# Optimization experiments

Hardware: AMD Instinct MI355X
Metric: run time of the kernel (lower is better)

Reference implementation:

```python
import jax, jax.numpy as jnp
import numpy as np

B, IN_C, H, W = 2, 256, 128, 128
KQ = 128            # kq_dim
K_LOCAL = 5         # subsample_local_ksize -> 25 local samples
S = 32              # subsample_num_samples (25 local + 7 random global)
STRIDES = (1, 2, 4) # levels 2, 3, 4


def _local_inds(h, w, k):
    # create_local_ind_buffer: flat index of the KxK window around each pixel,
    # coordinates clamped at the border (padding by replication).
    off = np.arange(k) - k // 2
    ii = np.clip(np.arange(h)[:, None] + off[None, :], 0, h - 1)  # [h,k]
    jj = np.clip(np.arange(w)[:, None] + off[None, :], 0, w - 1)  # [w,k]
    inds = ii[:, None, :, None] * w + jj[None, :, None, :]        # [h,w,k,k]
    return inds.reshape(h * w, k * k)


def setup_inputs() -> dict:
    key = jax.random.key(0)
    ks = jax.random.split(key, 4)
    rng = np.random.RandomState(0)
    inp = {
        'feats': jax.random.normal(ks[0], (B, IN_C, H, W), jnp.float32),
        'conv_w': jax.random.normal(ks[1], (KQ, IN_C, 3, 3), jnp.float32) * 0.02,
        'conv_b': jnp.zeros((KQ,), jnp.float32),
        'key_w': jax.random.normal(ks[2], (KQ, KQ), jnp.float32) * 0.05,
        'key_b': jnp.zeros((KQ,), jnp.float32),
        'query_w': jax.random.normal(ks[3], (KQ, KQ), jnp.float32) * 0.05,
        'query_b': jnp.zeros((KQ,), jnp.float32),
    }
    for lvl, s in zip((2, 3, 4), STRIDES):
        h, w = H // s, W // s
        n = h * w
        loc = np.broadcast_to(_local_inds(h, w, K_LOCAL)[None], (B, n, K_LOCAL * K_LOCAL))
        glob = rng.randint(0, n, size=(B, n, S - K_LOCAL * K_LOCAL))
        inp['sample_inds_%d' % lvl] = jnp.asarray(np.concatenate([loc, glob], -1), jnp.int32)
    return inp


def _pool(x, s):
    # utils.downscale_tensor: average-pool by the level stride
    if s == 1:
        return x
    b, c, h, w = x.shape
    return x.reshape(b, c, h // s, s, w // s, s).mean(axis=(3, 5))


def _level_logits(key_f, query_f, stride, inds):
    k = _pool(key_f, stride)
    q = _pool(query_f, stride)
    b, c, h, w = k.shape
    k = k.reshape(b, c, h * w).transpose(0, 2, 1)   # [B,N,C]
    q = q.reshape(b, c, h * w).transpose(0, 2, 1)   # [B,N,C]
    gk = k[jnp.arange(b)[:, None, None], inds]      # gather keys -> [B,N,S,C]
    # (gathered_query * gathered_key).sum(-1); query gather at node_inds is identity
    return jnp.einsum('bnc,bnsc->bns', q, gk) * (c ** -0.5)


def reference(feats, conv_w, conv_b, key_w, key_b, query_w, query_b,
              sample_inds_2, sample_inds_3, sample_inds_4):
    x = jax.lax.conv_general_dilated(
        feats, conv_w, (1, 1), 'SAME',
        dimension_numbers=('NCHW', 'OIHW', 'NCHW')) + conv_b[None, :, None, None]
    keys = jnp.einsum('bchw,kc->bkhw', x, key_w) + key_b[None, :, None, None]
    queries = jnp.einsum('bchw,kc->bkhw', x, query_w) + query_b[None, :, None, None]
    logits = [
        _level_logits(keys, queries, s, i)
        for s, i in zip(STRIDES, (sample_inds_2, sample_inds_3, sample_inds_4))
    ]
    # subsample_logits for levels 2/3/4, concatenated along the node dim
    return jnp.concatenate(logits, axis=1)  # [B, 16384+4096+1024, S]
```

## Files before the change

### kernel.cpp

```cpp
#include <hip/hip_runtime.h>
#include <cstddef>
#include <cstdint>

typedef __attribute__((ext_vector_type(8))) short short8;
typedef __attribute__((ext_vector_type(4))) float f32x4;

namespace {
constexpr int B_   = 2;
constexpr int HW   = 16384;
constexpr int NTOT = 21504;
constexpr float SCALE = 0.088388347648318447f;
}

__device__ __forceinline__ unsigned short f2bf(float f) {
    unsigned u = __builtin_bit_cast(unsigned, f);
    u += 0x7fffu + ((u >> 16) & 1u);
    return (unsigned short)(u >> 16);
}
__device__ __forceinline__ float bf2f(unsigned short h) {
    return __builtin_bit_cast(float, (unsigned)h << 16);
}
__device__ __forceinline__ float blo(unsigned u) {
    return __builtin_bit_cast(float, u << 16);
}
__device__ __forceinline__ float bhi(unsigned u) {
    return __builtin_bit_cast(float, u & 0xffff0000u);
}
__device__ __forceinline__ void gload_lds16(const void* g, void* l) {
    __builtin_amdgcn_global_load_lds(
        (const __attribute__((address_space(1))) void*)g,
        (__attribute__((address_space(3))) void*)l, 16, 0, 0);
}

__global__ __launch_bounds__(64) void zb_k(unsigned short* __restrict__ fpm)
{
    int bid = blockIdx.x;
    int b = bid >= 516;
    int i = bid - b * 516;
    int yy, xx;
    if (i < 130)      { yy = 0;       xx = i; }
    else if (i < 260) { yy = 129;     xx = i - 130; }
    else if (i < 388) { yy = i - 259; xx = 0; }
    else              { yy = i - 387; xx = 129; }
    ((unsigned long long*)fpm)[((size_t)(b * 130 + yy) * 130 + xx) * 64 + threadIdx.x] = 0ull;
}

__global__ __launch_bounds__(256) void t_k(
    const float* __restrict__ feats, unsigned short* __restrict__ fpm)
{
    __shared__ unsigned short ls[256 * 72];
    const int tid = threadIdx.x;
    const int b    = blockIdx.x >> 8;
    const int rem  = blockIdx.x & 255;
    const int y    = rem >> 1;
    const int gx0  = (rem & 1) << 6;

    const int cs = tid >> 4, x0 = (tid & 15) << 2;
#pragma unroll
    for (int j = 0; j < 16; ++j) {
        int c = (j << 4) + cs;
        float4 v = *(const float4*)&feats[(((size_t)b * 256 + c) << 14) + (y << 7) + gx0 + x0];
        uint2 pk;
        pk.x = (unsigned)f2bf(v.x) | ((unsigned)f2bf(v.y) << 16);
        pk.y = (unsigned)f2bf(v.z) | ((unsigned)f2bf(v.w) << 16);
        *(uint2*)&ls[c * 72 + x0] = pk;
    }
    __syncthreads();

    const int x = tid >> 2, q = tid & 3;
    unsigned short* orow = fpm +
        (((size_t)(b * 130 + y + 1) * 130) + 1 + gx0 + x) * 256 + (q << 6);
#pragma unroll
    for (int u = 0; u < 8; ++u) {
        int c0 = (q << 6) + (u << 3);
        unsigned w0 = (unsigned)ls[(c0 + 0) * 72 + x] | ((unsigned)ls[(c0 + 1) * 72 + x] << 16);
        unsigned w1 = (unsigned)ls[(c0 + 2) * 72 + x] | ((unsigned)ls[(c0 + 3) * 72 + x] << 16);
        unsigned w2 = (unsigned)ls[(c0 + 4) * 72 + x] | ((unsigned)ls[(c0 + 5) * 72 + x] << 16);
        unsigned w3 = (unsigned)ls[(c0 + 6) * 72 + x] | ((unsigned)ls[(c0 + 7) * 72 + x] << 16);
        uint4 o; o.x = w0; o.y = w1; o.z = w2; o.w = w3;
        *(uint4*)(orow + (u << 3)) = o;
    }
}

__global__ __launch_bounds__(256) void prep_w_k(
    const float* __restrict__ cw, const float* __restrict__ kw,
    const float* __restrict__ qw, unsigned short* __restrict__ wp)
{
    __shared__ float cvec[128][4];
    const int tid = threadIdx.x;
    const int g = blockIdx.x;
    for (int idx = tid; idx < 512; idx += 256) {
        int j = idx >> 2, q = idx & 3;
        int pair = (g << 2) + q;
        int c = pair / 9, tap = pair - c * 9;
        cvec[j][q] = cw[j * 2304 + c * 9 + tap];
    }
    __syncthreads();
    const int oc = tid & 127, isQ = tid >> 7;
    const float* wrow = (isQ ? qw : kw) + oc * 128;
    float acc0 = 0.f, acc1 = 0.f, acc2 = 0.f, acc3 = 0.f;
    for (int j = 0; j < 128; ++j) {
        float wv = wrow[j];
        acc0 += wv * cvec[j][0]; acc1 += wv * cvec[j][1];
        acc2 += wv * cvec[j][2]; acc3 += wv * cvec[j][3];
    }
    float accs[4] = {acc0, acc1, acc2, acc3};
#pragma unroll
    for (int q = 0; q < 4; ++q) {
        int pair = (g << 2) + q;
        int c = pair / 9, tap = pair - c * 9;
        int chunk = c >> 5, kg = (c >> 3) & 3, i = c & 7;
        int nf = (isQ << 3) + (oc >> 4);
        int lane = (kg << 4) + (oc & 15);
        wp[((size_t)(((chunk * 9 + tap) << 4) + nf) << 9) + (lane << 3) + i] = f2bf(accs[q]);
    }
}

__global__ __launch_bounds__(256) void prep_bias_k(
    const float* __restrict__ cb, const float* __restrict__ kw,
    const float* __restrict__ qw, const float* __restrict__ kb,
    const float* __restrict__ qb, float* __restrict__ bias)
{
    __shared__ float cbv[128];
    const int tid = threadIdx.x;
    if (tid < 128) cbv[tid] = cb[tid];
    __syncthreads();
    const int oc = tid & 127, isQ = tid >> 7;
    const float* wrow = (isQ ? qw : kw) + oc * 128;
    float a = isQ ? qb[oc] : kb[oc];
    for (int j = 0; j < 128; ++j) a += wrow[j] * cbv[j];
    bias[tid] = a;
}

__global__ __launch_bounds__(256, 2) void conv2_k(
    const unsigned short* __restrict__ fpm, const unsigned short* __restrict__ wp,
    const float* __restrict__ kqbias, unsigned short* __restrict__ kT,
    unsigned short* __restrict__ qT)
{
    __shared__ __align__(16) unsigned char abuf[2][7168];
    const int tid = threadIdx.x;
    const int w = tid >> 6, lane = tid & 63;
    const int raw = blockIdx.x;
    const int bid = ((raw & 7) << 6) + (raw >> 3);
    const int b = bid >> 8, tile = bid & 255;
    const int ty0 = (tile >> 4) << 3, tx0 = (tile & 15) << 3;
    const int r = lane & 15, g = lane >> 4;

    const int sp_sub = lane >> 2, sp_o = (lane & 3) << 4;
    const int pbase = (((r >> 3) * 10) + (r & 7)) * 64 + (g << 4);
    const unsigned char* wpB = (const unsigned char*)wp + ((w << 2) << 10) + (lane << 4);

    f32x4 acc[4][4];
#pragma unroll
    for (int mi = 0; mi < 4; ++mi)
#pragma unroll
        for (int ni = 0; ni < 4; ++ni) acc[mi][ni] = (f32x4){0.f, 0.f, 0.f, 0.f};

    auto stage = [&](int chunk, int buf) {
#pragma unroll
        for (int k = 0; k < 2; ++k) {
            int i = w + (k << 2);
            if (i < 7) {
                int pl0 = (i << 4) + sp_sub;
                int y = (pl0 * 6554) >> 16;
                int x = pl0 - y * 10;
                const unsigned char* src = (const unsigned char*)fpm +
                    (((size_t)((b * 130 + ty0 + y) * 130 + tx0 + x)) << 9) +
                    (chunk << 6) + sp_o;
                gload_lds16(src, &abuf[buf][i << 10]);
            }
        }
    };

    stage(0, 0);
    __syncthreads();

    for (int chunk = 0; chunk < 8; ++chunk) {
        const unsigned char* ab = abuf[chunk & 1];
        if (chunk < 7) stage(chunk + 1, (chunk + 1) & 1);
        const unsigned char* wbase = wpB + (size_t)chunk * 147456;

        short8 breg[2][4];
#pragma unroll
        for (int ni = 0; ni < 4; ++ni)
            breg[0][ni] = *(const short8*)(wbase + (ni << 10));

#pragma unroll
        for (int tap = 0; tap < 9; ++tap) {
            const int dy = tap / 3, dx = tap % 3;
            const int cur = tap & 1, nxt = cur ^ 1;
            if (tap < 8) {
#pragma unroll
                for (int ni = 0; ni < 4; ++ni)
                    breg[nxt][ni] = *(const short8*)(wbase + (tap + 1) * 16384 + (ni << 10));
            }
            short8 af[4];
#pragma unroll
            for (int mi = 0; mi < 4; ++mi)
                af[mi] = *(const short8*)(ab + pbase + (((2 * mi + dy) * 10 + dx) << 6));
#pragma unroll
            for (int mi = 0; mi < 4; ++mi)
#pragma unroll
                for (int ni = 0; ni < 4; ++ni)
                    acc[mi][ni] = __builtin_amdgcn_mfma_f32_16x16x32_bf16(
                        af[mi], breg[cur][ni], acc[mi][ni], 0, 0, 0);
        }
        __syncthreads();
    }

    const int col = lane & 15;
    const int mrow0 = g << 2;
#pragma unroll
    for (int ni = 0; ni < 4; ++ni) {
        int nf = (w << 2) + ni;
        unsigned short* dst = (nf < 8) ? kT : qT;
        int oc = ((nf & 7) << 4) + col;
        float bias = kqbias[(nf < 8 ? 0 : 128) + oc];
#pragma unroll
        for (int mi = 0; mi < 4; ++mi)
#pragma unroll
            for (int reg = 0; reg < 4; ++reg) {
                int m = mrow0 + reg;
                int ly = 2 * mi + (m >> 3), lx = m & 7;
                int gp = ((ty0 + ly) << 7) + tx0 + lx;
                dst[(((size_t)b << 14) + gp) * 128 + oc] = f2bf(acc[mi][ni][reg] + bias);
            }
    }
}

__global__ __launch_bounds__(256) void pool_all_k(
    const unsigned short* __restrict__ kT1, const unsigned short* __restrict__ qT1,
    unsigned short* __restrict__ kT2, unsigned short* __restrict__ qT2,
    unsigned short* __restrict__ kT3, unsigned short* __restrict__ qT3)
{
    const int bid = blockIdx.x;
    const unsigned short* src; unsigned short* dst;
    int s, pwshift, np, b, bx;
    if (bid < 2048) {
        int j = bid & 1023;
        src = (bid < 1024) ? kT1 : qT1; dst = (bid < 1024) ? kT2 : qT2;
        s = 2; pwshift = 6; np = 4096; b = j >> 9; bx = j & 511;
    } else {
        int j = (bid - 2048) & 255;
        src = (bid < 2304) ? kT1 : qT1; dst = (bid < 2304) ? kT3 : qT3;
        s = 4; pwshift = 5; np = 1024; b = j >> 7; bx = j & 127;
    }
    const int tid = threadIdx.x;
    const int pp = (bx << 3) + (tid >> 5);
    const int c4 = (tid & 31) << 2;
    const int ppy = pp >> pwshift, ppx = pp & ((1 << pwshift) - 1);
    float a0 = 0.f, a1 = 0.f, a2 = 0.f, a3 = 0.f;
    for (int sy = 0; sy < s; ++sy)
        for (int sx = 0; sx < s; ++sx) {
            int sp = ((ppy * s + sy) << 7) + ppx * s + sx;
            ushort4 v = *(const ushort4*)(src + (((size_t)b << 14) + sp) * 128 + c4);
            a0 += bf2f(v.x); a1 += bf2f(v.y); a2 += bf2f(v.z); a3 += bf2f(v.w);
        }
    const float inv = 1.f / (float)(s * s);
    ushort4 o;
    o.x = f2bf(a0 * inv); o.y = f2bf(a1 * inv);
    o.z = f2bf(a2 * inv); o.w = f2bf(a3 * inv);
    *(ushort4*)(dst + ((size_t)b * np + pp) * 128 + c4) = o;
}

__global__ __launch_bounds__(512, 2) void gdot_all_k(
    const unsigned short* __restrict__ qT1, const unsigned short* __restrict__ kT1,
    const unsigned short* __restrict__ qT2, const unsigned short* __restrict__ kT2,
    const unsigned short* __restrict__ qT3, const unsigned short* __restrict__ kT3,
    const int* __restrict__ i2, const int* __restrict__ i3, const int* __restrict__ i4,
    float* __restrict__ out)
{
    __shared__ __align__(16) unsigned char kwin[144 * 256];

    const int raw = blockIdx.x;
    const int bid = (raw & 7) * 84 + (raw >> 3);

    const unsigned short *qT, *kT;
    const int* inds;
    int n, wshift, tpbsh, twsh, off;
    if (bid < 512) {
        qT = qT1; kT = kT1; inds = i2; n = 16384; wshift = 7; tpbsh = 8; twsh = 4; off = 0;
    } else if (bid < 640) {
        qT = qT2; kT = kT2; inds = i3; n = 4096;  wshift = 6; tpbsh = 6; twsh = 3; off = 16384;
    } else {
        qT = qT3; kT = kT3; inds = i4; n = 1024;  wshift = 5; tpbsh = 4; twsh = 2; off = 20480;
    }
    const int lb   = bid - ((bid < 512) ? 0 : (bid < 640) ? 512 : 640);
    const int b    = lb >> tpbsh;
    const int tile = lb & ((1 << tpbsh) - 1);
    const int ty0  = (tile >> twsh) << 3;
    const int tx0  = (tile & ((1 << twsh) - 1)) << 3;
    const int W    = 1 << wshift, Wm1 = W - 1;
    const int ry0  = ty0 - 2, cx0 = tx0 - 2;

    const int tid   = threadIdx.x;
    const int pxl   = tid >> 3;
    const int slice = tid & 7;
    const int py = pxl >> 3, px = pxl & 7;
    const int nid = ((ty0 + py) << wshift) + tx0 + px;

    for (int idx = tid; idx < 2304; idx += 512) {
        int slot = idx >> 4, w16 = idx & 15;
        int sy = ry0 + slot / 12, sx = cx0 + slot % 12;
        sy = min(max(sy, 0), Wm1); sx = min(max(sx, 0), Wm1);
        uint4 v = *(const uint4*)(kT + ((size_t)(b * n + (sy << wshift) + sx) * 128) + (w16 << 3));
        *(uint4*)&kwin[slot * 256 + ((w16 ^ (slot & 7)) << 4)] = v;
    }

    float qr[16];
    {
        const uint4* qp = (const uint4*)(qT + ((size_t)(b * n + nid) * 128) + (slice << 4));
        uint4 q0 = qp[0], q1 = qp[1];
        qr[0] = blo(q0.x); qr[1] = bhi(q0.x); qr[2] = blo(q0.y); qr[3] = bhi(q0.y);
        qr[4] = blo(q0.z); qr[5] = bhi(q0.z); qr[6] = blo(q0.w); qr[7] = bhi(q0.w);
        qr[8] = blo(q1.x); qr[9] = bhi(q1.x); qr[10] = blo(q1.y); qr[11] = bhi(q1.y);
        qr[12] = blo(q1.z); qr[13] = bhi(q1.z); qr[14] = blo(q1.w); qr[15] = bhi(q1.w);
    }
    __syncthreads();

    const int* irow = inds + ((size_t)(b * n + nid) << 5);
    const int w2 = slice << 1;
    float* orow = out + (((size_t)b * NTOT + off + nid) << 5);

    for (int s = 0; s < 32; ++s) {
        int ind = irow[s];
        uint4 k0, k1;
        if (s < 25) {
            int iy = ind >> wshift, ix = ind & Wm1;
            int slot = (iy - ry0) * 12 + (ix - cx0);
            int sw = slot & 7;
            const unsigned char* base = kwin + slot * 256;
            k0 = *(const uint4*)(base + ((w2 ^ sw) << 4));
            k1 = *(const uint4*)(base + (((w2 + 1) ^ sw) << 4));
        } else {
            const uint4* kp = (const uint4*)(kT + ((size_t)(b * n + ind) * 128) + (slice << 4));
            k0 = kp[0]; k1 = kp[1];
        }
        float a = qr[0] * blo(k0.x) + qr[1] * bhi(k0.x)
                + qr[2] * blo(k0.y) + qr[3] * bhi(k0.y)
                + qr[4] * blo(k0.z) + qr[5] * bhi(k0.z)
                + qr[6] * blo(k0.w) + qr[7] * bhi(k0.w)
                + qr[8] * blo(k1.x) + qr[9] * bhi(k1.x)
                + qr[10] * blo(k1.y) + qr[11] * bhi(k1.y)
                + qr[12] * blo(k1.z) + qr[13] * bhi(k1.z)
                + qr[14] * blo(k1.w) + qr[15] * bhi(k1.w);
        a += __shfl_xor(a, 1);
        a += __shfl_xor(a, 2);
        a += __shfl_xor(a, 4);
        if (slice == 0) orow[s] = a * SCALE;
    }
}

extern "C" void kernel_launch(void* const* d_in, const int* in_sizes, int n_in,
                              void* d_out, int out_size, void* d_ws, size_t ws_size,
                              hipStream_t stream)
{
    const float* feats = (const float*)d_in[0];
    const float* cw    = (const float*)d_in[1];
    const float* cb    = (const float*)d_in[2];
    const float* kw    = (const float*)d_in[3];
    const float* kb    = (const float*)d_in[4];
    const float* qw    = (const float*)d_in[5];
    const float* qb    = (const float*)d_in[6];
    const int*   i2    = (const int*)d_in[7];
    const int*   i3    = (const int*)d_in[8];
    const int*   i4    = (const int*)d_in[9];
    float* out = (float*)d_out;

    char* ws = (char*)d_ws;
    unsigned short* wp   = (unsigned short*)ws;
    float*          bias = (float*)(ws + 1179648);
    unsigned short* fpm  = (unsigned short*)(ws + 1180672);
    unsigned short* kT1  = (unsigned short*)(ws + 18624512);
    unsigned short* qT1  = kT1 + 4194304;
    unsigned short* kT2  = qT1 + 4194304;
    unsigned short* qT2  = kT2 + 1048576;
    unsigned short* kT3  = qT2 + 1048576;
    unsigned short* qT3  = kT3 + 262144;

    zb_k<<<dim3(1032), 64, 0, stream>>>(fpm);
    t_k<<<dim3(512), 256, 0, stream>>>(feats, fpm);
    prep_w_k<<<dim3(576), 256, 0, stream>>>(cw, kw, qw, wp);
    prep_bias_k<<<dim3(1), 256, 0, stream>>>(cb, kw, qw, kb, qb, bias);
    conv2_k<<<dim3(512), 256, 0, stream>>>(fpm, wp, bias, kT1, qT1);
    pool_all_k<<<dim3(2560), 256, 0, stream>>>(kT1, qT1, kT2, qT2, kT3, qT3);
    gdot_all_k<<<dim3(672), 512, 0, stream>>>(qT1, kT1, qT2, kT2, qT3, kT3,
                                              i2, i3, i4, out);
}
```

Measured before the change: 212.2 us.

## Fuse pooling into conv epilogue, merge prep kernels, fold border zeroing into transpose

The separate border-zeroing, bias-prep and pooling kernels are removed. Zero padding moves into a new transpose kernel that reads the input directly without an LDS stage, and bias prep becomes an extra block of the weight-prep kernel. The conv kernel now stages its output tile in LDS, writes coalesced rows, and computes the 2x and 4x average pools from that tile. The gather-dot kernel preloads its index row and the random-global keys into registers and writes results as float4 from every slice. The weight register double-buffering, block swizzle and the 2-blocks-per-SM bound on gdot are also dropped, and the large extra LDS buffer in conv may lower occupancy.

```diff
diff --git a/kernel.cpp b/kernel.cpp
--- a/kernel.cpp
+++ b/kernel.cpp
@@ -26,68 +26,68 @@
 __device__ __forceinline__ float bhi(unsigned u) {
     return __builtin_bit_cast(float, u & 0xffff0000u);
 }
+__device__ __forceinline__ unsigned pk2(float a, float b) {
+    return (unsigned)f2bf(a) | ((unsigned)f2bf(b) << 16);
+}
 __device__ __forceinline__ void gload_lds16(const void* g, void* l) {
     __builtin_amdgcn_global_load_lds(
         (const __attribute__((address_space(1))) void*)g,
         (__attribute__((address_space(3))) void*)l, 16, 0, 0);
 }
 
-__global__ __launch_bounds__(64) void zb_k(unsigned short* __restrict__ fpm)
-{
-    int bid = blockIdx.x;
-    int b = bid >= 516;
-    int i = bid - b * 516;
-    int yy, xx;
-    if (i < 130)      { yy = 0;       xx = i; }
-    else if (i < 260) { yy = 129;     xx = i - 130; }
-    else if (i < 388) { yy = i - 259; xx = 0; }
-    else              { yy = i - 387; xx = 129; }
-    ((unsigned long long*)fpm)[((size_t)(b * 130 + yy) * 130 + xx) * 64 + threadIdx.x] = 0ull;
-}
-
-__global__ __launch_bounds__(256) void t_k(
+__global__ __launch_bounds__(256) void t2_k(
     const float* __restrict__ feats, unsigned short* __restrict__ fpm)
 {
-    __shared__ unsigned short ls[256 * 72];
     const int tid = threadIdx.x;
-    const int b    = blockIdx.x >> 8;
-    const int rem  = blockIdx.x & 255;
-    const int y    = rem >> 1;
-    const int gx0  = (rem & 1) << 6;
-
-    const int cs = tid >> 4, x0 = (tid & 15) << 2;
-#pragma unroll
-    for (int j = 0; j < 16; ++j) {
-        int c = (j << 4) + cs;
-        float4 v = *(const float4*)&feats[(((size_t)b * 256 + c) << 14) + (y << 7) + gx0 + x0];
-        uint2 pk;
-        pk.x = (unsigned)f2bf(v.x) | ((unsigned)f2bf(v.y) << 16);
-        pk.y = (unsigned)f2bf(v.z) | ((unsigned)f2bf(v.w) << 16);
-        *(uint2*)&ls[c * 72 + x0] = pk;
-    }
-    __syncthreads();
-
-    const int x = tid >> 2, q = tid & 3;
-    unsigned short* orow = fpm +
-        (((size_t)(b * 130 + y + 1) * 130) + 1 + gx0 + x) * 256 + (q << 6);
-#pragma unroll
-    for (int u = 0; u < 8; ++u) {
-        int c0 = (q << 6) + (u << 3);
-        unsigned w0 = (unsigned)ls[(c0 + 0) * 72 + x] | ((unsigned)ls[(c0 + 1) * 72 + x] << 16);
-        unsigned w1 = (unsigned)ls[(c0 + 2) * 72 + x] | ((unsigned)ls[(c0 + 3) * 72 + x] << 16);
-        unsigned w2 = (unsigned)ls[(c0 + 4) * 72 + x] | ((unsigned)ls[(c0 + 5) * 72 + x] << 16);
-        unsigned w3 = (unsigned)ls[(c0 + 6) * 72 + x] | ((unsigned)ls[(c0 + 7) * 72 + x] << 16);
-        uint4 o; o.x = w0; o.y = w1; o.z = w2; o.w = w3;
-        *(uint4*)(orow + (u << 3)) = o;
-    }
-}
-
-__global__ __launch_bounds__(256) void prep_w_k(
+    const int lane = tid & 63, cg = tid >> 6;
+    const int y = blockIdx.x >> 1, xseg = blockIdx.x & 1;
+    const int b = blockIdx.y;
+    const int x = (xseg << 6) + lane;
+    const bool inter = (y >= 1 && y <= 128);
+    const float* src = feats + (((size_t)b * 256) << 14) + ((y - 1) << 7) + x;
+    unsigned short* orow = fpm + ((size_t)(b * 130 + y) * 130 + 1 + x) * 256;
+
+#pragma unroll
+    for (int it = 0; it < 8; ++it) {
+        const int c0 = (it << 5) + (cg << 3);
+        uint4 v = {0u, 0u, 0u, 0u};
+        if (inter) {
+            float f0 = src[(size_t)(c0 + 0) << 14], f1 = src[(size_t)(c0 + 1) << 14];
+            float f2 = src[(size_t)(c0 + 2) << 14], f3 = src[(size_t)(c0 + 3) << 14];
+            float f4 = src[(size_t)(c0 + 4) << 14], f5 = src[(size_t)(c0 + 5) << 14];
+            float f6 = src[(size_t)(c0 + 6) << 14], f7 = src[(size_t)(c0 + 7) << 14];
+            v.x = pk2(f0, f1); v.y = pk2(f2, f3); v.z = pk2(f4, f5); v.w = pk2(f6, f7);
+        }
+        *(uint4*)(orow + c0) = v;
+    }
+    if (xseg == 0) {
+        uint4 z = {0u, 0u, 0u, 0u};
+        if (tid < 32)
+            *(uint4*)(fpm + ((size_t)(b * 130 + y) * 130 + 0) * 256 + (tid << 3)) = z;
+        else if (tid < 64)
+            *(uint4*)(fpm + ((size_t)(b * 130 + y) * 130 + 129) * 256 + ((tid - 32) << 3)) = z;
+    }
+}
+
+__global__ __launch_bounds__(256) void prep_k(
     const float* __restrict__ cw, const float* __restrict__ kw,
-    const float* __restrict__ qw, unsigned short* __restrict__ wp)
+    const float* __restrict__ qw, const float* __restrict__ cb,
+    const float* __restrict__ kb, const float* __restrict__ qb,
+    unsigned short* __restrict__ wp, float* __restrict__ bias)
 {
+    const int tid = threadIdx.x;
+    if (blockIdx.x == 576) {
+        __shared__ float cbv[128];
+        if (tid < 128) cbv[tid] = cb[tid];
+        __syncthreads();
+        const int oc = tid & 127, isQ = tid >> 7;
+        const float* wrow = (isQ ? qw : kw) + oc * 128;
+        float a = isQ ? qb[oc] : kb[oc];
+        for (int j = 0; j < 128; ++j) a += wrow[j] * cbv[j];
+        bias[tid] = a;
+        return;
+    }
     __shared__ float cvec[128][4];
-    const int tid = threadIdx.x;
     const int g = blockIdx.x;
     for (int idx = tid; idx < 512; idx += 256) {
         int j = idx >> 2, q = idx & 3;
@@ -116,32 +116,19 @@
     }
 }
 
-__global__ __launch_bounds__(256) void prep_bias_k(
-    const float* __restrict__ cb, const float* __restrict__ kw,
-    const float* __restrict__ qw, const float* __restrict__ kb,
-    const float* __restrict__ qb, float* __restrict__ bias)
-{
-    __shared__ float cbv[128];
-    const int tid = threadIdx.x;
-    if (tid < 128) cbv[tid] = cb[tid];
-    __syncthreads();
-    const int oc = tid & 127, isQ = tid >> 7;
-    const float* wrow = (isQ ? qw : kw) + oc * 128;
-    float a = isQ ? qb[oc] : kb[oc];
-    for (int j = 0; j < 128; ++j) a += wrow[j] * cbv[j];
-    bias[tid] = a;
-}
-
-__global__ __launch_bounds__(256, 2) void conv2_k(
+__global__ __launch_bounds__(256, 2) void conv3_k(
     const unsigned short* __restrict__ fpm, const unsigned short* __restrict__ wp,
     const float* __restrict__ kqbias, unsigned short* __restrict__ kT,
-    unsigned short* __restrict__ qT)
+    unsigned short* __restrict__ qT, unsigned short* __restrict__ kT2,
+    unsigned short* __restrict__ qT2, unsigned short* __restrict__ kT3,
+    unsigned short* __restrict__ qT3)
 {
     __shared__ __align__(16) unsigned char abuf[2][7168];
+    __shared__ __align__(16) unsigned short obuf[64 * 264];
+
     const int tid = threadIdx.x;
     const int w = tid >> 6, lane = tid & 63;
-    const int raw = blockIdx.x;
-    const int bid = ((raw & 7) << 6) + (raw >> 3);
+    const int bid = blockIdx.x;
     const int b = bid >> 8, tile = bid & 255;
     const int ty0 = (tile >> 4) << 3, tx0 = (tile & 15) << 3;
     const int r = lane & 15, g = lane >> 4;
@@ -179,21 +166,13 @@
         const unsigned char* ab = abuf[chunk & 1];
         if (chunk < 7) stage(chunk + 1, (chunk + 1) & 1);
         const unsigned char* wbase = wpB + (size_t)chunk * 147456;
-
-        short8 breg[2][4];
-#pragma unroll
-        for (int ni = 0; ni < 4; ++ni)
-            breg[0][ni] = *(const short8*)(wbase + (ni << 10));
-
 #pragma unroll
         for (int tap = 0; tap < 9; ++tap) {
             const int dy = tap / 3, dx = tap % 3;
-            const int cur = tap & 1, nxt = cur ^ 1;
-            if (tap < 8) {
-#pragma unroll
-                for (int ni = 0; ni < 4; ++ni)
-                    breg[nxt][ni] = *(const short8*)(wbase + (tap + 1) * 16384 + (ni << 10));
-            }
+            short8 bf[4];
+#pragma unroll
+            for (int ni = 0; ni < 4; ++ni)
+                bf[ni] = *(const short8*)(wbase + tap * 16384 + (ni << 10));
             short8 af[4];
 #pragma unroll
             for (int mi = 0; mi < 4; ++mi)
@@ -203,7 +182,7 @@
 #pragma unroll
                 for (int ni = 0; ni < 4; ++ni)
                     acc[mi][ni] = __builtin_amdgcn_mfma_f32_16x16x32_bf16(
-                        af[mi], breg[cur][ni], acc[mi][ni], 0, 0, 0);
+                        af[mi], bf[ni], acc[mi][ni], 0, 0, 0);
         }
         __syncthreads();
     }
@@ -212,58 +191,86 @@
     const int mrow0 = g << 2;
 #pragma unroll
     for (int ni = 0; ni < 4; ++ni) {
-        int nf = (w << 2) + ni;
-        unsigned short* dst = (nf < 8) ? kT : qT;
-        int oc = ((nf & 7) << 4) + col;
-        float bias = kqbias[(nf < 8 ? 0 : 128) + oc];
+        const int nf = (w << 2) + ni;
+        const float bv = kqbias[(nf << 4) + col];
 #pragma unroll
         for (int mi = 0; mi < 4; ++mi)
 #pragma unroll
             for (int reg = 0; reg < 4; ++reg) {
                 int m = mrow0 + reg;
-                int ly = 2 * mi + (m >> 3), lx = m & 7;
-                int gp = ((ty0 + ly) << 7) + tx0 + lx;
-                dst[(((size_t)b << 14) + gp) * 128 + oc] = f2bf(acc[mi][ni][reg] + bias);
+                int pxl = ((2 * mi + (m >> 3)) << 3) + (m & 7);
+                obuf[pxl * 264 + (nf << 4) + col] = f2bf(acc[mi][ni][reg] + bv);
             }
     }
-}
-
-__global__ __launch_bounds__(256) void pool_all_k(
-    const unsigned short* __restrict__ kT1, const unsigned short* __restrict__ qT1,
-    unsigned short* __restrict__ kT2, unsigned short* __restrict__ qT2,
-    unsigned short* __restrict__ kT3, unsigned short* __restrict__ qT3)
-{
-    const int bid = blockIdx.x;
-    const unsigned short* src; unsigned short* dst;
-    int s, pwshift, np, b, bx;
-    if (bid < 2048) {
-        int j = bid & 1023;
-        src = (bid < 1024) ? kT1 : qT1; dst = (bid < 1024) ? kT2 : qT2;
-        s = 2; pwshift = 6; np = 4096; b = j >> 9; bx = j & 511;
-    } else {
-        int j = (bid - 2048) & 255;
-        src = (bid < 2304) ? kT1 : qT1; dst = (bid < 2304) ? kT3 : qT3;
-        s = 4; pwshift = 5; np = 1024; b = j >> 7; bx = j & 127;
-    }
-    const int tid = threadIdx.x;
-    const int pp = (bx << 3) + (tid >> 5);
-    const int c4 = (tid & 31) << 2;
-    const int ppy = pp >> pwshift, ppx = pp & ((1 << pwshift) - 1);
-    float a0 = 0.f, a1 = 0.f, a2 = 0.f, a3 = 0.f;
-    for (int sy = 0; sy < s; ++sy)
-        for (int sx = 0; sx < s; ++sx) {
-            int sp = ((ppy * s + sy) << 7) + ppx * s + sx;
-            ushort4 v = *(const ushort4*)(src + (((size_t)b << 14) + sp) * 128 + c4);
-            a0 += bf2f(v.x); a1 += bf2f(v.y); a2 += bf2f(v.z); a3 += bf2f(v.w);
-        }
-    const float inv = 1.f / (float)(s * s);
-    ushort4 o;
-    o.x = f2bf(a0 * inv); o.y = f2bf(a1 * inv);
-    o.z = f2bf(a2 * inv); o.w = f2bf(a3 * inv);
-    *(ushort4*)(dst + ((size_t)b * np + pp) * 128 + c4) = o;
-}
-
-__global__ __launch_bounds__(512, 2) void gdot_all_k(
+    __syncthreads();
+
+    {
+        const int px = tid >> 2, q = tid & 3;
+        const int gp = ((ty0 + (px >> 3)) << 7) + tx0 + (px & 7);
+        const unsigned short* srow = obuf + px * 264 + (q << 6);
+        unsigned short* dp = (q < 2)
+            ? kT + ((((size_t)b << 14) + gp) << 7) + (q << 6)
+            : qT + ((((size_t)b << 14) + gp) << 7) + ((q - 2) << 6);
+#pragma unroll
+        for (int j = 0; j < 8; ++j)
+            *(uint4*)(dp + (j << 3)) = *(const uint4*)(srow + (j << 3));
+    }
+
+    {
+        const int pp = tid >> 4, ocg = tid & 15, oc0 = ocg << 4;
+        const int py2 = pp >> 2, px2 = pp & 3;
+        const int gp2 = (((ty0 >> 1) + py2) << 6) + (tx0 >> 1) + px2;
+        unsigned short* dp = (oc0 < 128)
+            ? kT2 + (((size_t)b * 4096 + gp2) << 7) + oc0
+            : qT2 + (((size_t)b * 4096 + gp2) << 7) + (oc0 - 128);
+#pragma unroll
+        for (int h = 0; h < 2; ++h) {
+            float s0=0,s1=0,s2=0,s3=0,s4=0,s5=0,s6=0,s7=0;
+#pragma unroll
+            for (int dy = 0; dy < 2; ++dy)
+#pragma unroll
+                for (int dx = 0; dx < 2; ++dx) {
+                    int pxl = (((py2 << 1) + dy) << 3) + (px2 << 1) + dx;
+                    uint4 v = *(const uint4*)(obuf + pxl * 264 + oc0 + (h << 3));
+                    s0 += blo(v.x); s1 += bhi(v.x); s2 += blo(v.y); s3 += bhi(v.y);
+                    s4 += blo(v.z); s5 += bhi(v.z); s6 += blo(v.w); s7 += bhi(v.w);
+                }
+            uint4 o;
+            o.x = pk2(s0 * 0.25f, s1 * 0.25f); o.y = pk2(s2 * 0.25f, s3 * 0.25f);
+            o.z = pk2(s4 * 0.25f, s5 * 0.25f); o.w = pk2(s6 * 0.25f, s7 * 0.25f);
+            *(uint4*)(dp + (h << 3)) = o;
+        }
+    }
+
+    if (tid < 64) {
+        const int pp = tid >> 4, ocg = tid & 15, oc0 = ocg << 4;
+        const int py4 = pp >> 1, px4 = pp & 1;
+        const int gp4 = (((ty0 >> 2) + py4) << 5) + (tx0 >> 2) + px4;
+        unsigned short* dp = (oc0 < 128)
+            ? kT3 + (((size_t)b * 1024 + gp4) << 7) + oc0
+            : qT3 + (((size_t)b * 1024 + gp4) << 7) + (oc0 - 128);
+#pragma unroll
+        for (int h = 0; h < 2; ++h) {
+            float s0=0,s1=0,s2=0,s3=0,s4=0,s5=0,s6=0,s7=0;
+#pragma unroll
+            for (int dy = 0; dy < 4; ++dy)
+#pragma unroll
+                for (int dx = 0; dx < 4; ++dx) {
+                    int pxl = (((py4 << 2) + dy) << 3) + (px4 << 2) + dx;
+                    uint4 v = *(const uint4*)(obuf + pxl * 264 + oc0 + (h << 3));
+                    s0 += blo(v.x); s1 += bhi(v.x); s2 += blo(v.y); s3 += bhi(v.y);
+                    s4 += blo(v.z); s5 += bhi(v.z); s6 += blo(v.w); s7 += bhi(v.w);
+                }
+            const float f = 0.0625f;
+            uint4 o;
+            o.x = pk2(s0 * f, s1 * f); o.y = pk2(s2 * f, s3 * f);
+            o.z = pk2(s4 * f, s5 * f); o.w = pk2(s6 * f, s7 * f);
+            *(uint4*)(dp + (h << 3)) = o;
+        }
+    }
+}
+
+__global__ __launch_bounds__(512) void gdot_all_k(
     const unsigned short* __restrict__ qT1, const unsigned short* __restrict__ kT1,
     const unsigned short* __restrict__ qT2, const unsigned short* __restrict__ kT2,
     const unsigned short* __restrict__ qT3, const unsigned short* __restrict__ kT3,
@@ -319,22 +326,40 @@
     __syncthreads();
 
     const int* irow = inds + ((size_t)(b * n + nid) << 5);
+    int ia[32];
+    {
+        const int4* ip = (const int4*)irow;
+#pragma unroll
+        for (int j = 0; j < 8; ++j) {
+            int4 v = ip[j];
+            ia[4 * j] = v.x; ia[4 * j + 1] = v.y; ia[4 * j + 2] = v.z; ia[4 * j + 3] = v.w;
+        }
+    }
+
+    uint4 rk0[7], rk1[7];
+#pragma unroll
+    for (int rr = 0; rr < 7; ++rr) {
+        const uint4* kp = (const uint4*)(kT + (((size_t)(b * n + ia[25 + rr])) << 7) + (slice << 4));
+        rk0[rr] = kp[0]; rk1[rr] = kp[1];
+    }
+
     const int w2 = slice << 1;
+    float res4[4] = {0.f, 0.f, 0.f, 0.f};
     float* orow = out + (((size_t)b * NTOT + off + nid) << 5);
 
+#pragma unroll
     for (int s = 0; s < 32; ++s) {
-        int ind = irow[s];
         uint4 k0, k1;
         if (s < 25) {
+            int ind = ia[s];
             int iy = ind >> wshift, ix = ind & Wm1;
             int slot = (iy - ry0) * 12 + (ix - cx0);
             int sw = slot & 7;
-            const unsigned char* base = kwin + slot * 256;
-            k0 = *(const uint4*)(base + ((w2 ^ sw) << 4));
-            k1 = *(const uint4*)(base + (((w2 + 1) ^ sw) << 4));
+            const unsigned char* base2 = kwin + slot * 256;
+            k0 = *(const uint4*)(base2 + ((w2 ^ sw) << 4));
+            k1 = *(const uint4*)(base2 + (((w2 + 1) ^ sw) << 4));
         } else {
-            const uint4* kp = (const uint4*)(kT + ((size_t)(b * n + ind) * 128) + (slice << 4));
-            k0 = kp[0]; k1 = kp[1];
+            k0 = rk0[s - 25]; k1 = rk1[s - 25];
         }
         float a = qr[0] * blo(k0.x) + qr[1] * bhi(k0.x)
                 + qr[2] * blo(k0.y) + qr[3] * bhi(k0.y)
@@ -347,8 +372,9 @@
         a += __shfl_xor(a, 1);
         a += __shfl_xor(a, 2);
         a += __shfl_xor(a, 4);
-        if (slice == 0) orow[s] = a * SCALE;
-    }
+        if ((s >> 2) == slice) res4[s & 3] = a * SCALE;
+    }
+    *(float4*)(orow + (slice << 2)) = *(const float4*)res4;
 }
 
 extern "C" void kernel_launch(void* const* d_in, const int* in_sizes, int n_in,
@@ -378,12 +404,10 @@
     unsigned short* kT3  = qT2 + 1048576;
     unsigned short* qT3  = kT3 + 262144;
 
-    zb_k<<<dim3(1032), 64, 0, stream>>>(fpm);
-    t_k<<<dim3(512), 256, 0, stream>>>(feats, fpm);
-    prep_w_k<<<dim3(576), 256, 0, stream>>>(cw, kw, qw, wp);
-    prep_bias_k<<<dim3(1), 256, 0, stream>>>(cb, kw, qw, kb, qb, bias);
-    conv2_k<<<dim3(512), 256, 0, stream>>>(fpm, wp, bias, kT1, qT1);
-    pool_all_k<<<dim3(2560), 256, 0, stream>>>(kT1, qT1, kT2, qT2, kT3, qT3);
+    t2_k<<<dim3(260, 2), 256, 0, stream>>>(feats, fpm);
+    prep_k<<<dim3(577), 256, 0, stream>>>(cw, kw, qw, cb, kb, qb, wp, bias);
+    conv3_k<<<dim3(512), 256, 0, stream>>>(fpm, wp, bias, kT1, qT1,
+                                           kT2, qT2, kT3, qT3);
     gdot_all_k<<<dim3(672), 512, 0, stream>>>(qT1, kT1, qT2, kT2, qT3, kT3,
                                               i2, i3, i4, out);
 }
```

Measured after the change: 186.9 us. 1.14x faster.
